# Performance work log

Measured on AMD Instinct MI355X. Metric: run time of the kernel, lower is better.

The kernel has to match this reference:

```python
import jax, jax.numpy as jnp
import numpy as np

NUM_GROUPS = 8


def setup_inputs() -> dict:
    key = jax.random.key(0)
    k1, k2, k3, k4 = jax.random.split(key, 4)
    N, D_IN, D_OUT = 16384, 2048, 2048
    x = jax.random.normal(k1, (N, D_IN), dtype=jnp.float32)
    # kaiming-uniform-ish scale for weight, uniform bound for bias (values only need realistic scale)
    bound_w = 1.0 / np.sqrt(D_IN)
    weight = jax.random.uniform(k2, (NUM_GROUPS, D_OUT, D_IN), minval=-bound_w, maxval=bound_w, dtype=jnp.float32)
    bias = jax.random.uniform(k3, (NUM_GROUPS, D_OUT), minval=-bound_w, maxval=bound_w, dtype=jnp.float32)
    group_indices = jnp.sort(jax.random.randint(k4, (N,), 0, NUM_GROUPS, dtype=jnp.int32))
    return {"x": x, "weight": weight, "bias": bias, "group_indices": group_indices}


def reference(x, weight, bias, group_indices):
    """Grouped linear: out[n] = x[n] @ weight[g[n]].T + bias[g[n]].

    group_indices is sorted, so this matches the torch fallback's
    per-group gather + linear + concat row order exactly.
    """
    num_groups = weight.shape[0]
    out = jnp.zeros((x.shape[0], weight.shape[1]), dtype=x.dtype)
    for g in range(num_groups):  # fixed small loop over experts
        sel = (group_indices == g)[:, None]  # [N,1]
        # one dense GEMM per group, masked accumulate (rows not in group contribute 0)
        yg = jnp.matmul(x, weight[g].T) + bias[g]
        out = out + jnp.where(sel, yg, jnp.zeros((), dtype=x.dtype))
    return out
```

## Files before the change

kernel.cpp:

```cpp
#include <hip/hip_runtime.h>
#include <stdint.h>

#define N_ROWS 16384
#define K_DIM  2048
#define N_OUT  2048
#define NGROUPS 8
#define BM 256
#define BN 256
#define BK 64
#define MAX_Y 72

typedef short s16x8 __attribute__((ext_vector_type(8)));
typedef float f32x4 __attribute__((ext_vector_type(4)));

__device__ __forceinline__ unsigned short f2bf(float f) {
    unsigned int u = __float_as_uint(f);
    u += 0x7fffu + ((u >> 16) & 1u);
    return (unsigned short)(u >> 16);
}

__global__ void convert_kernel(const float* __restrict__ src,
                               unsigned short* __restrict__ dst, int n) {
    int stride = gridDim.x * blockDim.x;
    for (int i = blockIdx.x * blockDim.x + threadIdx.x; i * 4 < n; i += stride) {
        float4 v = *(const float4*)(src + (size_t)i * 4);
        ushort4 o;
        o.x = f2bf(v.x); o.y = f2bf(v.y); o.z = f2bf(v.z); o.w = f2bf(v.w);
        *(ushort4*)(dst + (size_t)i * 4) = o;
    }
}

__device__ __forceinline__ int lower_bound_g(const int* __restrict__ gi, int g) {
    int lo = 0, hi = N_ROWS;
    while (lo < hi) { int mid = (lo + hi) >> 1; if (gi[mid] < g) lo = mid + 1; else hi = mid; }
    return lo;
}

#define GLDS16(gp, lp) \
    __builtin_amdgcn_global_load_lds((__attribute__((address_space(1))) void*)(gp), \
                                     (__attribute__((address_space(3))) void*)(lp), 16, 0, 0)

#define VMW(N)  asm volatile("s_waitcnt vmcnt(" #N ")" ::: "memory")
#define BAR()   asm volatile("s_barrier" ::: "memory")
#define LGKM0() do { asm volatile("s_waitcnt lgkmcnt(0)" ::: "memory"); \
                     __builtin_amdgcn_sched_barrier(0); } while (0)

__global__ __launch_bounds__(512, 2) void grouped_gemm(
    const unsigned short* __restrict__ xb,
    const unsigned short* __restrict__ wb,
    const float* __restrict__ bias,
    const int* __restrict__ gi,
    float* __restrict__ out)
{
    __shared__ unsigned char lds[131072];
    __shared__ int sh_s[NGROUPS + 1];

    const int t5 = threadIdx.x;

    if (t5 <= NGROUPS)
        sh_s[t5] = (t5 == 0) ? 0 : (t5 == NGROUPS ? N_ROWS : lower_bound_g(gi, t5));
    __syncthreads();

    int by = blockIdx.y;
    int row0 = -1, g = 0, nrows = 0, c = 0;
    #pragma unroll
    for (int gg = 0; gg < NGROUPS; gg++) {
        int n = sh_s[gg + 1] - sh_s[gg];
        int tiles = (n + BM - 1) >> 8;
        if (row0 < 0 && by < c + tiles) {
            g = gg;
            row0 = sh_s[gg] + (by - c) * BM;
            nrows = n - (by - c) * BM; if (nrows > BM) nrows = BM;
        }
        c += tiles;
    }
    if (row0 < 0) return;
    int col0 = blockIdx.x * BN;

    int rsub = t5 >> 2;
    int swz  = (t5 & 3) ^ ((rsub >> 1) & 3);
    int ar0 = min(row0 + rsub,       N_ROWS - 1);
    int ar1 = min(row0 + 128 + rsub, N_ROWS - 1);
    const unsigned short* srcA0 = xb + (size_t)ar0 * K_DIM + swz * 8;
    const unsigned short* srcA1 = xb + (size_t)ar1 * K_DIM + swz * 8;
    const unsigned short* srcB0 = wb + ((size_t)g * N_OUT + col0 + rsub) * K_DIM + swz * 8;
    const unsigned short* srcB1 = srcB0 + (size_t)128 * K_DIM;
    char* ldsA = (char*)lds;
    char* ldsB = (char*)lds + 65536;
    char* dA = ldsA + t5 * 16;
    char* dB = ldsB + t5 * 16;

#define STAGE_A(BUF,H,KT) do { \
    GLDS16(srcA0 + (KT)*64 + (H)*32, dA + (BUF)*32768 + (H)*16384); \
    GLDS16(srcA1 + (KT)*64 + (H)*32, dA + (BUF)*32768 + (H)*16384 + 8192); } while (0)
#define STAGE_B(BUF,H,KT) do { \
    GLDS16(srcB0 + (KT)*64 + (H)*32, dB + (BUF)*32768 + (H)*16384); \
    GLDS16(srcB1 + (KT)*64 + (H)*32, dB + (BUF)*32768 + (H)*16384 + 8192); } while (0)

    int w = t5 >> 6, l = t5 & 63, la = l & 15, q = l >> 4;
    int wm = w >> 2, wn = w & 3;
    int swr   = (q ^ ((la >> 1) & 3)) * 16;
    int aOff0 = (wm * 128 + la) * 64 + swr;
    int bOff0 = (wn * 64  + la) * 64 + swr;

#define RDA8(DST, BUF, KS) do { _Pragma("unroll") \
    for (int mi = 0; mi < 8; mi++) \
        DST[mi] = *(const s16x8*)(ldsA + (BUF)*32768 + (KS)*16384 + aOff0 + mi*1024); } while (0)
#define RDB1(DST, BUF, KS, NI) \
    DST = *(const s16x8*)(ldsB + (BUF)*32768 + (KS)*16384 + bOff0 + (NI)*1024)

    f32x4 acc[8][4];
    #pragma unroll
    for (int i2 = 0; i2 < 8; i2++)
        #pragma unroll
        for (int j2 = 0; j2 < 4; j2++)
            acc[i2][j2] = (f32x4){0.f, 0.f, 0.f, 0.f};

    s16x8 a0[8], a1[8], b0[4], b1[4];

#define MFMA16(AF, BL, BH, N0, N1) do { \
    __builtin_amdgcn_s_setprio(1); \
    _Pragma("unroll") for (int mi = 0; mi < 8; mi++) { \
        acc[mi][N0] = __builtin_amdgcn_mfma_f32_16x16x32_bf16(AF[mi], BL, acc[mi][N0], 0, 0, 0); \
        acc[mi][N1] = __builtin_amdgcn_mfma_f32_16x16x32_bf16(AF[mi], BH, acc[mi][N1], 0, 0, 0); } \
    __builtin_amdgcn_s_setprio(0); } while (0)

#define QTILE(BUF, ST1, ST2, ST3, ST4, W4) do { \
    RDA8(a0, BUF, 0); RDB1(b0[0], BUF, 0, 0); RDB1(b0[1], BUF, 0, 1); \
    ST1; BAR(); LGKM0(); MFMA16(a0, b0[0], b0[1], 0, 1); BAR(); \
    RDB1(b0[2], BUF, 0, 2); RDB1(b0[3], BUF, 0, 3); \
    ST2; BAR(); LGKM0(); MFMA16(a0, b0[2], b0[3], 2, 3); BAR(); \
    RDA8(a1, BUF, 1); RDB1(b1[0], BUF, 1, 0); RDB1(b1[1], BUF, 1, 1); \
    ST3; BAR(); LGKM0(); MFMA16(a1, b1[0], b1[1], 0, 1); BAR(); \
    RDB1(b1[2], BUF, 1, 2); RDB1(b1[3], BUF, 1, 3); \
    ST4; W4; BAR(); LGKM0(); MFMA16(a1, b1[2], b1[3], 2, 3); BAR(); \
} while (0)

    STAGE_A(0,0,0); STAGE_B(0,0,0); STAGE_A(0,1,0); STAGE_B(0,1,0);
    STAGE_A(1,0,1); STAGE_B(1,0,1); STAGE_A(1,1,1);
    VMW(6);
    BAR();

    #pragma unroll 1
    for (int i = 0; i < 15; i++) {
        int kt0 = 2 * i + 2, kt1 = 2 * i + 3, ktp = 2 * i + 1;
        QTILE(0, STAGE_B(1,1,ktp), STAGE_A(0,0,kt0), STAGE_B(0,0,kt0),
                 STAGE_A(0,1,kt0), VMW(6));
        QTILE(1, STAGE_B(0,1,kt0), STAGE_A(1,0,kt1), STAGE_B(1,0,kt1),
                 STAGE_A(1,1,kt1), VMW(6));
    }
    QTILE(0, STAGE_B(1,1,31), ((void)0), ((void)0), ((void)0), VMW(0));
    QTILE(1, ((void)0), ((void)0), ((void)0), ((void)0), ((void)0));

    int row_end = row0 + nrows;
    float bv[4];
    #pragma unroll
    for (int ni = 0; ni < 4; ni++)
        bv[ni] = bias[g * N_OUT + col0 + wn * 64 + ni * 16 + la];
    #pragma unroll
    for (int mi = 0; mi < 8; mi++) {
        int rbase = row0 + wm * 128 + mi * 16 + q * 4;
        #pragma unroll
        for (int r = 0; r < 4; r++) {
            int row = rbase + r;
            if (row < row_end) {
                float* op = out + (size_t)row * N_OUT + col0 + wn * 64 + la;
                #pragma unroll
                for (int ni = 0; ni < 4; ni++)
                    op[ni * 16] = acc[mi][ni][r] + bv[ni];
            }
        }
    }
}

__global__ void naive_kernel(const float* __restrict__ x, const float* __restrict__ wgt,
                             const float* __restrict__ bias, const int* __restrict__ gi,
                             float* __restrict__ out) {
    int row = blockIdx.x;
    int g = gi[row] & (NGROUPS - 1);
    __shared__ float xs[K_DIM];
    for (int i = threadIdx.x; i < K_DIM; i += 256) xs[i] = x[(size_t)row * K_DIM + i];
    __syncthreads();
    for (int c = threadIdx.x; c < N_OUT; c += 256) {
        const float* wr = wgt + ((size_t)g * N_OUT + c) * K_DIM;
        float s = 0.f;
        for (int k = 0; k < K_DIM; k++) s += xs[k] * wr[k];
        out[(size_t)row * N_OUT + c] = s + bias[g * N_OUT + c];
    }
}

extern "C" void kernel_launch(void* const* d_in, const int* in_sizes, int n_in,
                              void* d_out, int out_size, void* d_ws, size_t ws_size,
                              hipStream_t stream) {
    const float* x    = (const float*)d_in[0];
    const float* wgt  = (const float*)d_in[1];
    const float* bias = (const float*)d_in[2];
    const int*   gi   = (const int*)d_in[3];
    float* out = (float*)d_out;

    const size_t xb_bytes = (size_t)N_ROWS * K_DIM * 2;
    const size_t wb_bytes = (size_t)NGROUPS * N_OUT * K_DIM * 2;
    const size_t need = xb_bytes + wb_bytes;

    if (ws_size < need) {
        naive_kernel<<<dim3(N_ROWS), dim3(256), 0, stream>>>(x, wgt, bias, gi, out);
        return;
    }

    unsigned short* xb = (unsigned short*)d_ws;
    unsigned short* wb = (unsigned short*)((char*)d_ws + xb_bytes);

    convert_kernel<<<dim3(8192), dim3(256), 0, stream>>>(x,   xb, N_ROWS * K_DIM);
    convert_kernel<<<dim3(8192), dim3(256), 0, stream>>>(wgt, wb, NGROUPS * N_OUT * K_DIM);
    grouped_gemm<<<dim3(N_OUT / BN, MAX_Y), dim3(512), 0, stream>>>(
        xb, wb, bias, gi, out);
}
```

Before: 494.4 us.

## Restructure GEMM main loop into triple-buffered BK=32 pipeline with register prefetch

Rewrites the grouped GEMM main loop to use BK=32 tiles in a three-stage LDS ring (96KB instead of 128KB) with even/odd register fragment double-buffering. LDS reads for the next tile are issued before the current MFMAs, using partial lgkmcnt waits instead of full drains and fewer barriers per tile. The conversion kernel is also widened to 8 elements per thread. This aims to hide LDS and global latency better, at the cost of redundant clamped loads at the tail and more register pressure.

```diff
diff --git a/kernel.cpp b/kernel.cpp
--- a/kernel.cpp
+++ b/kernel.cpp
@@ -7,10 +7,12 @@
 #define NGROUPS 8
 #define BM 256
 #define BN 256
-#define BK 64
+#define BK 32
+#define NT 64
 #define MAX_Y 72
 
 typedef short s16x8 __attribute__((ext_vector_type(8)));
+typedef unsigned short u16x8 __attribute__((ext_vector_type(8)));
 typedef float f32x4 __attribute__((ext_vector_type(4)));
 
 __device__ __forceinline__ unsigned short f2bf(float f) {
@@ -22,11 +24,13 @@
 __global__ void convert_kernel(const float* __restrict__ src,
                                unsigned short* __restrict__ dst, int n) {
     int stride = gridDim.x * blockDim.x;
-    for (int i = blockIdx.x * blockDim.x + threadIdx.x; i * 4 < n; i += stride) {
-        float4 v = *(const float4*)(src + (size_t)i * 4);
-        ushort4 o;
-        o.x = f2bf(v.x); o.y = f2bf(v.y); o.z = f2bf(v.z); o.w = f2bf(v.w);
-        *(ushort4*)(dst + (size_t)i * 4) = o;
+    for (int i = blockIdx.x * blockDim.x + threadIdx.x; i * 8 < n; i += stride) {
+        float4 v0 = *(const float4*)(src + (size_t)i * 8);
+        float4 v1 = *(const float4*)(src + (size_t)i * 8 + 4);
+        u16x8 o;
+        o[0] = f2bf(v0.x); o[1] = f2bf(v0.y); o[2] = f2bf(v0.z); o[3] = f2bf(v0.w);
+        o[4] = f2bf(v1.x); o[5] = f2bf(v1.y); o[6] = f2bf(v1.z); o[7] = f2bf(v1.w);
+        *(u16x8*)(dst + (size_t)i * 8) = o;
     }
 }
 
@@ -40,10 +44,11 @@
     __builtin_amdgcn_global_load_lds((__attribute__((address_space(1))) void*)(gp), \
                                      (__attribute__((address_space(3))) void*)(lp), 16, 0, 0)
 
-#define VMW(N)  asm volatile("s_waitcnt vmcnt(" #N ")" ::: "memory")
 #define BAR()   asm volatile("s_barrier" ::: "memory")
-#define LGKM0() do { asm volatile("s_waitcnt lgkmcnt(0)" ::: "memory"); \
+#define LGKM6() do { asm volatile("s_waitcnt lgkmcnt(6)" ::: "memory"); \
                      __builtin_amdgcn_sched_barrier(0); } while (0)
+#define VMW2()  asm volatile("s_waitcnt vmcnt(2)" ::: "memory")
+#define KEEP(x) asm volatile("" :: "v"(x))
 
 __global__ __launch_bounds__(512, 2) void grouped_gemm(
     const unsigned short* __restrict__ xb,
@@ -52,13 +57,13 @@
     const int* __restrict__ gi,
     float* __restrict__ out)
 {
-    __shared__ unsigned char lds[131072];
+    __shared__ unsigned char lds[98304];
     __shared__ int sh_s[NGROUPS + 1];
 
-    const int t5 = threadIdx.x;
-
-    if (t5 <= NGROUPS)
-        sh_s[t5] = (t5 == 0) ? 0 : (t5 == NGROUPS ? N_ROWS : lower_bound_g(gi, t5));
+    const int t = threadIdx.x;
+
+    if (t <= NGROUPS)
+        sh_s[t] = (t == 0) ? 0 : (t == NGROUPS ? N_ROWS : lower_bound_g(gi, t));
     __syncthreads();
 
     int by = blockIdx.y;
@@ -77,37 +82,34 @@
     if (row0 < 0) return;
     int col0 = blockIdx.x * BN;
 
-    int rsub = t5 >> 2;
-    int swz  = (t5 & 3) ^ ((rsub >> 1) & 3);
+    int rsub = t >> 2;
+    int swz  = (t & 3) ^ ((rsub >> 1) & 3);
     int ar0 = min(row0 + rsub,       N_ROWS - 1);
     int ar1 = min(row0 + 128 + rsub, N_ROWS - 1);
     const unsigned short* srcA0 = xb + (size_t)ar0 * K_DIM + swz * 8;
     const unsigned short* srcA1 = xb + (size_t)ar1 * K_DIM + swz * 8;
     const unsigned short* srcB0 = wb + ((size_t)g * N_OUT + col0 + rsub) * K_DIM + swz * 8;
     const unsigned short* srcB1 = srcB0 + (size_t)128 * K_DIM;
-    char* ldsA = (char*)lds;
-    char* ldsB = (char*)lds + 65536;
-    char* dA = ldsA + t5 * 16;
-    char* dB = ldsB + t5 * 16;
-
-#define STAGE_A(BUF,H,KT) do { \
-    GLDS16(srcA0 + (KT)*64 + (H)*32, dA + (BUF)*32768 + (H)*16384); \
-    GLDS16(srcA1 + (KT)*64 + (H)*32, dA + (BUF)*32768 + (H)*16384 + 8192); } while (0)
-#define STAGE_B(BUF,H,KT) do { \
-    GLDS16(srcB0 + (KT)*64 + (H)*32, dB + (BUF)*32768 + (H)*16384); \
-    GLDS16(srcB1 + (KT)*64 + (H)*32, dB + (BUF)*32768 + (H)*16384 + 8192); } while (0)
-
-    int w = t5 >> 6, l = t5 & 63, la = l & 15, q = l >> 4;
+    char* dA = (char*)lds + t * 16;
+    char* dB = (char*)lds + 49152 + t * 16;
+
+#define STG_A(OFF, KT) do { \
+    GLDS16(srcA0 + (KT) * 32, dA + (OFF)); \
+    GLDS16(srcA1 + (KT) * 32, dA + (OFF) + 8192); } while (0)
+#define STG_B(OFF, KT) do { \
+    GLDS16(srcB0 + (KT) * 32, dB + (OFF)); \
+    GLDS16(srcB1 + (KT) * 32, dB + (OFF) + 8192); } while (0)
+
+    int w = t >> 6, l = t & 63, la = l & 15, q = l >> 4;
     int wm = w >> 2, wn = w & 3;
-    int swr   = (q ^ ((la >> 1) & 3)) * 16;
-    int aOff0 = (wm * 128 + la) * 64 + swr;
-    int bOff0 = (wn * 64  + la) * 64 + swr;
-
-#define RDA8(DST, BUF, KS) do { _Pragma("unroll") \
-    for (int mi = 0; mi < 8; mi++) \
-        DST[mi] = *(const s16x8*)(ldsA + (BUF)*32768 + (KS)*16384 + aOff0 + mi*1024); } while (0)
-#define RDB1(DST, BUF, KS, NI) \
-    DST = *(const s16x8*)(ldsB + (BUF)*32768 + (KS)*16384 + bOff0 + (NI)*1024)
+    int swr = (q ^ ((la >> 1) & 3)) * 16;
+    const char* ldsAr = (const char*)lds;
+    const char* ldsBr = (const char*)lds + 49152;
+    int aBase = (wm * 128 + la) * 64 + swr;
+    int bBase = (wn * 64  + la) * 64 + swr;
+
+#define RDA(DST, OFF, MI) DST = *(const s16x8*)(ldsAr + (OFF) + aBase + (MI) * 1024)
+#define RDB(DST, OFF, NI) DST = *(const s16x8*)(ldsBr + (OFF) + bBase + (NI) * 1024)
 
     f32x4 acc[8][4];
     #pragma unroll
@@ -116,41 +118,61 @@
         for (int j2 = 0; j2 < 4; j2++)
             acc[i2][j2] = (f32x4){0.f, 0.f, 0.f, 0.f};
 
-    s16x8 a0[8], a1[8], b0[4], b1[4];
-
-#define MFMA16(AF, BL, BH, N0, N1) do { \
+    s16x8 aE[8], aO[8], bE[4], bO[4];
+    int oA0 = 0, oA1 = 16384, oA2 = 32768;
+    int oB0 = 0, oB1 = 16384, oB2 = 32768;
+
+#define MF2(AC, BL, BH, N0, N1) do { \
     __builtin_amdgcn_s_setprio(1); \
     _Pragma("unroll") for (int mi = 0; mi < 8; mi++) { \
-        acc[mi][N0] = __builtin_amdgcn_mfma_f32_16x16x32_bf16(AF[mi], BL, acc[mi][N0], 0, 0, 0); \
-        acc[mi][N1] = __builtin_amdgcn_mfma_f32_16x16x32_bf16(AF[mi], BH, acc[mi][N1], 0, 0, 0); } \
+        acc[mi][N0] = __builtin_amdgcn_mfma_f32_16x16x32_bf16(AC[mi], BL, acc[mi][N0], 0, 0, 0); \
+        acc[mi][N1] = __builtin_amdgcn_mfma_f32_16x16x32_bf16(AC[mi], BH, acc[mi][N1], 0, 0, 0); } \
     __builtin_amdgcn_s_setprio(0); } while (0)
 
-#define QTILE(BUF, ST1, ST2, ST3, ST4, W4) do { \
-    RDA8(a0, BUF, 0); RDB1(b0[0], BUF, 0, 0); RDB1(b0[1], BUF, 0, 1); \
-    ST1; BAR(); LGKM0(); MFMA16(a0, b0[0], b0[1], 0, 1); BAR(); \
-    RDB1(b0[2], BUF, 0, 2); RDB1(b0[3], BUF, 0, 3); \
-    ST2; BAR(); LGKM0(); MFMA16(a0, b0[2], b0[3], 2, 3); BAR(); \
-    RDA8(a1, BUF, 1); RDB1(b1[0], BUF, 1, 0); RDB1(b1[1], BUF, 1, 1); \
-    ST3; BAR(); LGKM0(); MFMA16(a1, b1[0], b1[1], 0, 1); BAR(); \
-    RDB1(b1[2], BUF, 1, 2); RDB1(b1[3], BUF, 1, 3); \
-    ST4; W4; BAR(); LGKM0(); MFMA16(a1, b1[2], b1[3], 2, 3); BAR(); \
+#define TILE(AC, AN, BC, BN_, OA1_, OB0_, OB1_, OB2S, OA0S, KB, KA) do { \
+     \
+    RDB(BC[2], OB0_, 2); RDB(BC[3], OB0_, 3); \
+    RDA(AN[0], OA1_, 0); RDA(AN[1], OA1_, 1); RDA(AN[2], OA1_, 2); RDA(AN[3], OA1_, 3); \
+    LGKM6(); \
+    MF2(AC, BC[0], BC[1], 0, 1); \
+    VMW2(); BAR(); \
+    STG_B(OB2S, KB); \
+     \
+    RDA(AN[4], OA1_, 4); RDA(AN[5], OA1_, 5); RDA(AN[6], OA1_, 6); RDA(AN[7], OA1_, 7); \
+    RDB(BN_[0], OB1_, 0); RDB(BN_[1], OB1_, 1); \
+    LGKM6(); \
+    MF2(AC, BC[2], BC[3], 2, 3); \
+    VMW2(); BAR(); \
+    STG_A(OA0S, KA); \
 } while (0)
 
-    STAGE_A(0,0,0); STAGE_B(0,0,0); STAGE_A(0,1,0); STAGE_B(0,1,0);
-    STAGE_A(1,0,1); STAGE_B(1,0,1); STAGE_A(1,1,1);
-    VMW(6);
+    STG_A(oA0, 0); STG_B(oB0, 0); STG_A(oA1, 1);
+    STG_B(oB1, 1); STG_A(oA2, 2);
+    asm volatile("s_waitcnt vmcnt(4)" ::: "memory");
     BAR();
+    RDA(aE[0], oA0, 0); RDA(aE[1], oA0, 1); RDA(aE[2], oA0, 2); RDA(aE[3], oA0, 3);
+    RDA(aE[4], oA0, 4); RDA(aE[5], oA0, 5); RDA(aE[6], oA0, 6); RDA(aE[7], oA0, 7);
+    RDB(bE[0], oB0, 0); RDB(bE[1], oB0, 1);
 
     #pragma unroll 1
-    for (int i = 0; i < 15; i++) {
-        int kt0 = 2 * i + 2, kt1 = 2 * i + 3, ktp = 2 * i + 1;
-        QTILE(0, STAGE_B(1,1,ktp), STAGE_A(0,0,kt0), STAGE_B(0,0,kt0),
-                 STAGE_A(0,1,kt0), VMW(6));
-        QTILE(1, STAGE_B(0,1,kt0), STAGE_A(1,0,kt1), STAGE_B(1,0,kt1),
-                 STAGE_A(1,1,kt1), VMW(6));
-    }
-    QTILE(0, STAGE_B(1,1,31), ((void)0), ((void)0), ((void)0), VMW(0));
-    QTILE(1, ((void)0), ((void)0), ((void)0), ((void)0), ((void)0));
+    for (int i = 0; i < NT / 2; i++) {
+        int tE = 2 * i;
+        int kB0 = min(tE + 2, NT - 1), kA0 = min(tE + 3, NT - 1);
+        int kB1 = min(tE + 3, NT - 1), kA1 = min(tE + 4, NT - 1);
+        TILE(aE, aO, bE, bO, oA1, oB0, oB1, oB2, oA0, kB0, kA0);
+        int tmp = oA0; oA0 = oA1; oA1 = oA2; oA2 = tmp;
+        tmp = oB0; oB0 = oB1; oB1 = oB2; oB2 = tmp;
+        TILE(aO, aE, bO, bE, oA1, oB0, oB1, oB2, oA0, kB1, kA1);
+        tmp = oA0; oA0 = oA1; oA1 = oA2; oA2 = tmp;
+        tmp = oB0; oB0 = oB1; oB1 = oB2; oB2 = tmp;
+    }
+    asm volatile("s_waitcnt vmcnt(0)" ::: "memory");
+    __builtin_amdgcn_sched_barrier(0);
+
+    #pragma unroll
+    for (int i2 = 0; i2 < 8; i2++) { KEEP(aE[i2]); KEEP(aO[i2]); }
+    #pragma unroll
+    for (int i2 = 0; i2 < 4; i2++) { KEEP(bE[i2]); KEEP(bO[i2]); }
 
     int row_end = row0 + nrows;
     float bv[4];
```

Result: slower. 591.2 us (+19.6%).
